# Kernel tuning notes

Hardware: AMD Instinct MI355X
Metric: run time of the kernel (lower is better)

The kernel has to match this reference:

```python
import jax, jax.numpy as jnp
import numpy as np

IN_DIM = 768
OUT_DIM = 128
N_NODES = 100000
N_EDGES = 1600000


def setup_inputs() -> dict:
    key = jax.random.key(0)
    ks = jax.random.split(key, 9)
    features = jax.random.normal(ks[0], (N_NODES, IN_DIM), dtype=jnp.float32)
    src = jax.random.randint(ks[1], (N_EDGES,), 0, N_NODES, dtype=jnp.int32)
    dst = jax.random.randint(ks[2], (N_EDGES,), 0, N_NODES, dtype=jnp.int32)
    s = 1.0 / np.sqrt(IN_DIM)
    Wd = jax.random.uniform(ks[3], (IN_DIM, OUT_DIM), jnp.float32, -s, s)
    bd = jax.random.uniform(ks[4], (OUT_DIM,), jnp.float32, -s, s)
    sg = 1.0 / np.sqrt(OUT_DIM)
    Wg = jax.random.uniform(ks[5], (OUT_DIM, OUT_DIM), jnp.float32, -sg, sg)
    bg = jnp.zeros((OUT_DIM,), jnp.float32)  # DGL GraphConv bias init: zeros
    Wu = jax.random.uniform(ks[6], (OUT_DIM, 768), jnp.float32, -sg, sg)
    bu = jax.random.uniform(ks[7], (768,), jnp.float32, -sg, sg)
    return {"features": features, "Wd": Wd, "bd": bd, "Wg": Wg, "bg": bg,
            "Wu": Wu, "bu": bu, "src": src, "dst": dst}


def reference(features, Wd, bd, Wg, bg, Wu, bu, src, dst):
    # down-projection: [N, in_dim] -> [N, out_dim]
    h = features @ Wd + bd

    # DGL GraphConv, norm='both': D_in^{-1/2} A D_out^{-1/2} (h W) + b
    ones = jnp.ones_like(src, dtype=h.dtype)
    out_deg = jax.ops.segment_sum(ones, src, num_segments=N_NODES)
    in_deg = jax.ops.segment_sum(ones, dst, num_segments=N_NODES)
    norm_src = jax.lax.rsqrt(jnp.maximum(out_deg, 1.0))  # clamp(min=1)
    norm_dst = jax.lax.rsqrt(jnp.maximum(in_deg, 1.0))

    # in_feats == out_feats -> aggregate first, then multiply by Wg
    h = h * norm_src[:, None]
    agg = jax.ops.segment_sum(h[src], dst, num_segments=N_NODES)  # [N, out_dim]
    agg = agg * norm_dst[:, None]
    g = agg @ Wg + bg

    # up-projection back to 768
    return g @ Wu + bu
```

## Files before the change

kernel.cpp:

```cpp
#include <hip/hip_runtime.h>
#include <cstdint>
#include <cstddef>

#define IN_DIM 768
#define OUT_DIM 128
#define N_NODES 100000
#define N_EDGES 1600000

typedef __bf16 bf16x8 __attribute__((ext_vector_type(8)));
typedef float f32x4 __attribute__((ext_vector_type(4)));

static __device__ __forceinline__ unsigned short f2bf(float f) {
  unsigned u = __builtin_bit_cast(unsigned, f);
  u += 0x7fffu + ((u >> 16) & 1u);
  return (unsigned short)(u >> 16);
}
static __device__ __forceinline__ float bflo(unsigned u) {
  return __builtin_bit_cast(float, u << 16);
}
static __device__ __forceinline__ float bfhi(unsigned u) {
  return __builtin_bit_cast(float, u & 0xffff0000u);
}


__global__ void deg_kernel(const int* __restrict__ src, const int* __restrict__ dst,
                           int* __restrict__ out_deg, int* __restrict__ in_deg) {
  int e = blockIdx.x * 256 + threadIdx.x;
  if (e < N_EDGES) {
    atomicAdd(&out_deg[src[e]], 1);
    atomicAdd(&in_deg[dst[e]], 1);
  }
}

__global__ void norm_kernel(const int* __restrict__ out_deg, float* __restrict__ norm_src) {
  int i = blockIdx.x * 256 + threadIdx.x;
  if (i < N_NODES) norm_src[i] = rsqrtf(fmaxf((float)out_deg[i], 1.0f));
}

__global__ __launch_bounds__(256) void scanA_kernel(const int* __restrict__ in_deg,
                                                    int* __restrict__ row_start,
                                                    int* __restrict__ blk_sums) {
  __shared__ int sm[256];
  const int tid = threadIdx.x;
  const int base = blockIdx.x * 1024;
  int idx = base + tid * 4;
  int v0 = (idx + 0 < N_NODES) ? in_deg[idx + 0] : 0;
  int v1 = (idx + 1 < N_NODES) ? in_deg[idx + 1] : 0;
  int v2 = (idx + 2 < N_NODES) ? in_deg[idx + 2] : 0;
  int v3 = (idx + 3 < N_NODES) ? in_deg[idx + 3] : 0;
  int t0 = v0, t1 = t0 + v1, t2 = t1 + v2, t3 = t2 + v3;
  sm[tid] = t3;
  __syncthreads();
  for (int off = 1; off < 256; off <<= 1) {
    int x = (tid >= off) ? sm[tid - off] : 0;
    __syncthreads();
    sm[tid] += x;
    __syncthreads();
  }
  int base_sum = tid ? sm[tid - 1] : 0;
  if (idx + 0 < N_NODES) row_start[idx + 0] = base_sum;
  if (idx + 1 < N_NODES) row_start[idx + 1] = base_sum + t0;
  if (idx + 2 < N_NODES) row_start[idx + 2] = base_sum + t1;
  if (idx + 3 < N_NODES) row_start[idx + 3] = base_sum + t2;
  if (tid == 255) blk_sums[blockIdx.x] = sm[255];
}

__global__ void scanB_kernel(const int* __restrict__ blk_sums, int* __restrict__ blk_off) {
  __shared__ int sm[128];
  const int tid = threadIdx.x;
  const int nblk = (N_NODES + 1023) / 1024;
  int v = (tid < nblk) ? blk_sums[tid] : 0;
  sm[tid] = v;
  __syncthreads();
  for (int off = 1; off < 128; off <<= 1) {
    int x = (tid >= off) ? sm[tid - off] : 0;
    __syncthreads();
    sm[tid] += x;
    __syncthreads();
  }
  blk_off[tid] = tid ? sm[tid - 1] : 0;
}

__global__ void scanC_kernel(int* __restrict__ row_start, const int* __restrict__ blk_off,
                             int* __restrict__ cursor) {
  int i = blockIdx.x * 256 + threadIdx.x;
  if (i < N_NODES) {
    int v = row_start[i] + blk_off[i >> 10];
    row_start[i] = v;
    cursor[i] = v;
  }
  if (i == 0) row_start[N_NODES] = N_EDGES;
}

__global__ void scatter_kernel(const int* __restrict__ src, const int* __restrict__ dst,
                               int* __restrict__ cursor, int* __restrict__ edge_src) {
  int e = blockIdx.x * 256 + threadIdx.x;
  if (e < N_EDGES) {
    int p = atomicAdd(&cursor[dst[e]], 1);
    edge_src[p] = src[e];
  }
}


__global__ void wdt_kernel(const float* __restrict__ Wd, unsigned short* __restrict__ WdT) {
  int n = blockIdx.x;
  int k = threadIdx.x;
  WdT[(size_t)n * IN_DIM + k] = f2bf(Wd[(size_t)k * OUT_DIM + n]);
}


__global__ __launch_bounds__(256) void gemm1_kernel(
    const float* __restrict__ feat, const unsigned short* __restrict__ WdT,
    const float* __restrict__ bd, const float* __restrict__ norm_src,
    unsigned short* __restrict__ hbf) {
  __shared__ unsigned short a_lds[64][72];
  __shared__ unsigned short b_lds[128][72];
  const int tid = threadIdx.x;
  const int wave = tid >> 6;
  const int lane = tid & 63;
  const int mrow = (wave >> 1) * 32;
  const int ncol = (wave & 1) * 64;
  const int block_m = blockIdx.x * 64;
  const int fm = lane & 15;
  const int fq = lane >> 4;

  f32x4 acc[2][4] = {};

  for (int k0 = 0; k0 < IN_DIM; k0 += 64) {
#pragma unroll
    for (int p = 0; p < 4; ++p) {
      int idx = tid + p * 256;
      int r = idx >> 4;
      int c4 = (idx & 15) * 4;
      int gr = block_m + r;
      float4 v;
      if (gr < N_NODES) v = *(const float4*)(feat + (size_t)gr * IN_DIM + k0 + c4);
      else v = make_float4(0.f, 0.f, 0.f, 0.f);
      ushort4 s;
      s.x = f2bf(v.x); s.y = f2bf(v.y); s.z = f2bf(v.z); s.w = f2bf(v.w);
      *(ushort4*)&a_lds[r][c4] = s;
    }
#pragma unroll
    for (int p = 0; p < 4; ++p) {
      int idx = tid + p * 256;
      int n = idx >> 3;
      int ch = (idx & 7) * 8;
      uint4 v = *(const uint4*)(WdT + (size_t)n * IN_DIM + k0 + ch);
      *(uint4*)&b_lds[n][ch] = v;
    }
    __syncthreads();
#pragma unroll
    for (int ks = 0; ks < 64; ks += 32) {
      int kc = ks + fq * 8;
      bf16x8 af[2], bfr[4];
      af[0] = *(const bf16x8*)&a_lds[mrow + fm][kc];
      af[1] = *(const bf16x8*)&a_lds[mrow + 16 + fm][kc];
#pragma unroll
      for (int i = 0; i < 4; ++i)
        bfr[i] = *(const bf16x8*)&b_lds[ncol + i * 16 + fm][kc];
#pragma unroll
      for (int mi = 0; mi < 2; ++mi)
#pragma unroll
        for (int ni = 0; ni < 4; ++ni)
          acc[mi][ni] = __builtin_amdgcn_mfma_f32_16x16x32_bf16(af[mi], bfr[ni], acc[mi][ni], 0, 0, 0);
    }
    __syncthreads();
  }
  const int fr = fq * 4;
#pragma unroll
  for (int mi = 0; mi < 2; ++mi) {
#pragma unroll
    for (int r = 0; r < 4; ++r) {
      int row = block_m + mrow + mi * 16 + fr + r;
      if (row < N_NODES) {
        float ns = norm_src[row];
#pragma unroll
        for (int ni = 0; ni < 4; ++ni) {
          int col = ncol + ni * 16 + fm;
          float val = (acc[mi][ni][r] + bd[col]) * ns;
          hbf[(size_t)row * OUT_DIM + col] = f2bf(val);
        }
      }
    }
  }
}


__global__ __launch_bounds__(256) void agg_kernel(
    const unsigned short* __restrict__ hbf, const int* __restrict__ row_start,
    const int* __restrict__ edge_src, unsigned short* __restrict__ aggb) {
  const int wave = threadIdx.x >> 6;
  const int lane = threadIdx.x & 63;
  const int v = blockIdx.x * 4 + wave;
  if (v >= N_NODES) return;
  const int beg = row_start[v];
  const int end = row_start[v + 1];
  const unsigned* hp = (const unsigned*)hbf;
  float a0 = 0.f, a1 = 0.f;
  for (int c = beg; c < end; c += 64) {
    int rem = end - c;
    int n = rem < 64 ? rem : 64;
    int sv = (c + lane < end) ? edge_src[c + lane] : 0;
    int j = 0;
    for (; j + 4 <= n; j += 4) {
      int s0 = __shfl(sv, j + 0);
      int s1 = __shfl(sv, j + 1);
      int s2 = __shfl(sv, j + 2);
      int s3 = __shfl(sv, j + 3);
      unsigned u0 = hp[(size_t)s0 * 64 + lane];
      unsigned u1 = hp[(size_t)s1 * 64 + lane];
      unsigned u2 = hp[(size_t)s2 * 64 + lane];
      unsigned u3 = hp[(size_t)s3 * 64 + lane];
      a0 += (bflo(u0) + bflo(u1)) + (bflo(u2) + bflo(u3));
      a1 += (bfhi(u0) + bfhi(u1)) + (bfhi(u2) + bfhi(u3));
    }
    for (; j < n; ++j) {
      int s = __shfl(sv, j);
      unsigned u = hp[(size_t)s * 64 + lane];
      a0 += bflo(u);
      a1 += bfhi(u);
    }
  }
  float nd = rsqrtf(fmaxf((float)(end - beg), 1.0f));
  a0 *= nd; a1 *= nd;
  unsigned o = (unsigned)f2bf(a0) | ((unsigned)f2bf(a1) << 16);
  ((unsigned*)aggb)[(size_t)v * 64 + lane] = o;
}


__global__ void wgu_kernel(const float* __restrict__ Wg, const float* __restrict__ Wu,
                           unsigned short* __restrict__ WguT) {
  int i = blockIdx.x * 256 + threadIdx.x;
  if (i >= 128 * 768) return;
  int r = i / 768, c = i % 768;
  float s = 0.f;
  for (int k = 0; k < 128; ++k) s += Wg[r * 128 + k] * Wu[(size_t)k * 768 + c];
  WguT[(size_t)c * 128 + r] = f2bf(s);
}

__global__ void bgu_kernel(const float* __restrict__ bg, const float* __restrict__ Wu,
                           const float* __restrict__ bu, float* __restrict__ bgu) {
  int c = blockIdx.x * 256 + threadIdx.x;
  if (c >= 768) return;
  float s = bu[c];
  for (int k = 0; k < 128; ++k) s += bg[k] * Wu[(size_t)k * 768 + c];
  bgu[c] = s;
}


__global__ __launch_bounds__(256) void gemm3_kernel(
    const unsigned short* __restrict__ aggb, const unsigned short* __restrict__ WguT,
    const float* __restrict__ bgu, float* __restrict__ out) {
  __shared__ unsigned short a_lds[128][72];
  __shared__ unsigned short b_lds[128][72];
  const int tid = threadIdx.x;
  const int wave = tid >> 6;
  const int lane = tid & 63;
  const int m_off = (wave >> 1) * 64;
  const int n_off = (wave & 1) * 64;
  const int block_m = blockIdx.x * 128;
  const int block_n = blockIdx.y * 128;
  const int fm = lane & 15;
  const int fq = lane >> 4;

  f32x4 acc[4][4] = {};

  for (int k0 = 0; k0 < 128; k0 += 64) {
#pragma unroll
    for (int p = 0; p < 4; ++p) {
      int idx = tid + p * 256;
      int r = idx >> 3, ch = idx & 7;
      int gr = block_m + r;
      uint4 v;
      if (gr < N_NODES) v = *(const uint4*)(aggb + (size_t)gr * 128 + k0 + ch * 8);
      else v = make_uint4(0u, 0u, 0u, 0u);
      *(uint4*)&a_lds[r][ch * 8] = v;
    }
#pragma unroll
    for (int p = 0; p < 4; ++p) {
      int idx = tid + p * 256;
      int n = idx >> 3, ch = idx & 7;
      uint4 v = *(const uint4*)(WguT + (size_t)(block_n + n) * 128 + k0 + ch * 8);
      *(uint4*)&b_lds[n][ch * 8] = v;
    }
    __syncthreads();
#pragma unroll
    for (int ks = 0; ks < 64; ks += 32) {
      bf16x8 af[4], bfr[4];
      int kc = ks + fq * 8;
#pragma unroll
      for (int i = 0; i < 4; ++i) af[i] = *(const bf16x8*)&a_lds[m_off + i * 16 + fm][kc];
#pragma unroll
      for (int i = 0; i < 4; ++i) bfr[i] = *(const bf16x8*)&b_lds[n_off + i * 16 + fm][kc];
#pragma unroll
      for (int mi = 0; mi < 4; ++mi)
#pragma unroll
        for (int ni = 0; ni < 4; ++ni)
          acc[mi][ni] = __builtin_amdgcn_mfma_f32_16x16x32_bf16(af[mi], bfr[ni], acc[mi][ni], 0, 0, 0);
    }
    __syncthreads();
  }
  const int fr = fq * 4;
#pragma unroll
  for (int mi = 0; mi < 4; ++mi) {
#pragma unroll
    for (int r = 0; r < 4; ++r) {
      int row = block_m + m_off + mi * 16 + fr + r;
      if (row < N_NODES) {
#pragma unroll
        for (int ni = 0; ni < 4; ++ni) {
          int col = block_n + n_off + ni * 16 + fm;
          out[(size_t)row * IN_DIM + col] = acc[mi][ni][r] + bgu[col];
        }
      }
    }
  }
}


extern "C" void kernel_launch(void* const* d_in, const int* in_sizes, int n_in,
                              void* d_out, int out_size, void* d_ws, size_t ws_size,
                              hipStream_t stream) {
  (void)in_sizes; (void)n_in; (void)out_size; (void)ws_size;
  const float* feat = (const float*)d_in[0];
  const float* Wd   = (const float*)d_in[1];
  const float* bd   = (const float*)d_in[2];
  const float* Wg   = (const float*)d_in[3];
  const float* bg   = (const float*)d_in[4];
  const float* Wu   = (const float*)d_in[5];
  const float* bu   = (const float*)d_in[6];
  const int*   src  = (const int*)d_in[7];
  const int*   dst  = (const int*)d_in[8];
  float* out = (float*)d_out;

  char* ws = (char*)d_ws;
  unsigned short* hbf       = (unsigned short*)(ws + 0);
  unsigned short* aggb      = (unsigned short*)(ws + 25600000);
  int*            edge_srcs = (int*)(ws + 51200000);
  int*            out_deg   = (int*)(ws + 57600000);
  int*            in_deg    = (int*)(ws + 58000000);
  int*            row_start = (int*)(ws + 58400000);
  int*            cursor    = (int*)(ws + 58800128);
  float*          norm_src  = (float*)(ws + 59200128);
  unsigned short* WguT      = (unsigned short*)(ws + 59600128);
  float*          bgu       = (float*)(ws + 59796736);
  unsigned short* WdT       = (unsigned short*)(ws + 59799808);
  int*            blk_sums  = (int*)(ws + 59996416);
  int*            blk_off   = (int*)(ws + 59996928);

  hipMemsetAsync(out_deg, 0, 800000, stream);
  deg_kernel<<<(N_EDGES + 255) / 256, 256, 0, stream>>>(src, dst, out_deg, in_deg);
  norm_kernel<<<(N_NODES + 255) / 256, 256, 0, stream>>>(out_deg, norm_src);
  scanA_kernel<<<(N_NODES + 1023) / 1024, 256, 0, stream>>>(in_deg, row_start, blk_sums);
  scanB_kernel<<<1, 128, 0, stream>>>(blk_sums, blk_off);
  scanC_kernel<<<(N_NODES + 255) / 256, 256, 0, stream>>>(row_start, blk_off, cursor);
  scatter_kernel<<<(N_EDGES + 255) / 256, 256, 0, stream>>>(src, dst, cursor, edge_srcs);
  wdt_kernel<<<128, 768, 0, stream>>>(Wd, WdT);
  gemm1_kernel<<<(N_NODES + 63) / 64, 256, 0, stream>>>(feat, WdT, bd, norm_src, hbf);
  agg_kernel<<<(N_NODES + 3) / 4, 256, 0, stream>>>(hbf, row_start, edge_srcs, aggb);
  wgu_kernel<<<(128 * 768 + 255) / 256, 256, 0, stream>>>(Wg, Wu, WguT);
  bgu_kernel<<<3, 256, 0, stream>>>(bg, Wu, bu, bgu);
  gemm3_kernel<<<dim3((N_NODES + 127) / 128, 6), 256, 0, stream>>>(aggb, WguT, bgu, out);
}
```

Before: 926.5 us.

## Prefetch global tiles into registers in GEMMs, widen gather unroll, remap gemm3 across XCDs

gemm1 and gemm3 now load the next K tile from global memory into registers while the current tile is used from LDS, which hides load latency. The agg kernel gathers 8 neighbour rows per step with predicated weights, replacing the 4-way loop plus scalar tail. gemm3 moves to a 1D grid whose block IDs are remapped so that consecutive tiles land on the same XCD, improving L2 locality. norm_kernel is dropped and the source norm is computed inline from out_deg in gemm1's epilogue. The price is more register pressure and some redundant loads on short tail chunks in agg.

```diff
diff --git a/kernel.cpp b/kernel.cpp
--- a/kernel.cpp
+++ b/kernel.cpp
@@ -30,11 +30,6 @@
     atomicAdd(&out_deg[src[e]], 1);
     atomicAdd(&in_deg[dst[e]], 1);
   }
-}
-
-__global__ void norm_kernel(const int* __restrict__ out_deg, float* __restrict__ norm_src) {
-  int i = blockIdx.x * 256 + threadIdx.x;
-  if (i < N_NODES) norm_src[i] = rsqrtf(fmaxf((float)out_deg[i], 1.0f));
 }
 
 __global__ __launch_bounds__(256) void scanA_kernel(const int* __restrict__ in_deg,
@@ -111,7 +106,7 @@
 
 __global__ __launch_bounds__(256) void gemm1_kernel(
     const float* __restrict__ feat, const unsigned short* __restrict__ WdT,
-    const float* __restrict__ bd, const float* __restrict__ norm_src,
+    const float* __restrict__ bd, const int* __restrict__ out_deg,
     unsigned short* __restrict__ hbf) {
   __shared__ unsigned short a_lds[64][72];
   __shared__ unsigned short b_lds[128][72];
@@ -124,31 +119,48 @@
   const int fm = lane & 15;
   const int fq = lane >> 4;
 
+  const int ar = tid >> 4;
+  const int ac4 = (tid & 15) * 4;
+  const int bn = tid >> 3;
+  const int bch = (tid & 7) * 8;
+
   f32x4 acc[2][4] = {};
+  float4 av[4];
+  uint4 bv[4];
+
+#pragma unroll
+  for (int p = 0; p < 4; ++p) {
+    int gr = block_m + ar + p * 16;
+    av[p] = (gr < N_NODES) ? *(const float4*)(feat + (size_t)gr * IN_DIM + ac4)
+                           : make_float4(0.f, 0.f, 0.f, 0.f);
+  }
+#pragma unroll
+  for (int p = 0; p < 4; ++p)
+    bv[p] = *(const uint4*)(WdT + (size_t)(bn + p * 32) * IN_DIM + bch);
 
   for (int k0 = 0; k0 < IN_DIM; k0 += 64) {
 #pragma unroll
     for (int p = 0; p < 4; ++p) {
-      int idx = tid + p * 256;
-      int r = idx >> 4;
-      int c4 = (idx & 15) * 4;
-      int gr = block_m + r;
-      float4 v;
-      if (gr < N_NODES) v = *(const float4*)(feat + (size_t)gr * IN_DIM + k0 + c4);
-      else v = make_float4(0.f, 0.f, 0.f, 0.f);
       ushort4 s;
-      s.x = f2bf(v.x); s.y = f2bf(v.y); s.z = f2bf(v.z); s.w = f2bf(v.w);
-      *(ushort4*)&a_lds[r][c4] = s;
-    }
-#pragma unroll
-    for (int p = 0; p < 4; ++p) {
-      int idx = tid + p * 256;
-      int n = idx >> 3;
-      int ch = (idx & 7) * 8;
-      uint4 v = *(const uint4*)(WdT + (size_t)n * IN_DIM + k0 + ch);
-      *(uint4*)&b_lds[n][ch] = v;
-    }
-    __syncthreads();
+      s.x = f2bf(av[p].x); s.y = f2bf(av[p].y); s.z = f2bf(av[p].z); s.w = f2bf(av[p].w);
+      *(ushort4*)&a_lds[ar + p * 16][ac4] = s;
+    }
+#pragma unroll
+    for (int p = 0; p < 4; ++p)
+      *(uint4*)&b_lds[bn + p * 32][bch] = bv[p];
+    __syncthreads();
+    int kn = k0 + 64;
+    if (kn < IN_DIM) {
+#pragma unroll
+      for (int p = 0; p < 4; ++p) {
+        int gr = block_m + ar + p * 16;
+        av[p] = (gr < N_NODES) ? *(const float4*)(feat + (size_t)gr * IN_DIM + kn + ac4)
+                               : make_float4(0.f, 0.f, 0.f, 0.f);
+      }
+#pragma unroll
+      for (int p = 0; p < 4; ++p)
+        bv[p] = *(const uint4*)(WdT + (size_t)(bn + p * 32) * IN_DIM + kn + bch);
+    }
 #pragma unroll
     for (int ks = 0; ks < 64; ks += 32) {
       int kc = ks + fq * 8;
@@ -173,7 +185,7 @@
     for (int r = 0; r < 4; ++r) {
       int row = block_m + mrow + mi * 16 + fr + r;
       if (row < N_NODES) {
-        float ns = norm_src[row];
+        float ns = rsqrtf(fmaxf((float)out_deg[row], 1.0f));
 #pragma unroll
         for (int ni = 0; ni < 4; ++ni) {
           int col = ncol + ni * 16 + fm;
@@ -201,24 +213,40 @@
     int rem = end - c;
     int n = rem < 64 ? rem : 64;
     int sv = (c + lane < end) ? edge_src[c + lane] : 0;
-    int j = 0;
-    for (; j + 4 <= n; j += 4) {
-      int s0 = __shfl(sv, j + 0);
-      int s1 = __shfl(sv, j + 1);
-      int s2 = __shfl(sv, j + 2);
-      int s3 = __shfl(sv, j + 3);
+    int l = n - 1;
+    for (int j = 0; j < n; j += 8) {
+      int j1 = j + 1, j2 = j + 2, j3 = j + 3, j4 = j + 4, j5 = j + 5, j6 = j + 6, j7 = j + 7;
+      int s0 = __shfl(sv, j);
+      int s1 = __shfl(sv, j1 < n ? j1 : l);
+      int s2 = __shfl(sv, j2 < n ? j2 : l);
+      int s3 = __shfl(sv, j3 < n ? j3 : l);
+      int s4 = __shfl(sv, j4 < n ? j4 : l);
+      int s5 = __shfl(sv, j5 < n ? j5 : l);
+      int s6 = __shfl(sv, j6 < n ? j6 : l);
+      int s7 = __shfl(sv, j7 < n ? j7 : l);
       unsigned u0 = hp[(size_t)s0 * 64 + lane];
       unsigned u1 = hp[(size_t)s1 * 64 + lane];
       unsigned u2 = hp[(size_t)s2 * 64 + lane];
       unsigned u3 = hp[(size_t)s3 * 64 + lane];
-      a0 += (bflo(u0) + bflo(u1)) + (bflo(u2) + bflo(u3));
-      a1 += (bfhi(u0) + bfhi(u1)) + (bfhi(u2) + bfhi(u3));
-    }
-    for (; j < n; ++j) {
-      int s = __shfl(sv, j);
-      unsigned u = hp[(size_t)s * 64 + lane];
-      a0 += bflo(u);
-      a1 += bfhi(u);
+      unsigned u4 = hp[(size_t)s4 * 64 + lane];
+      unsigned u5 = hp[(size_t)s5 * 64 + lane];
+      unsigned u6 = hp[(size_t)s6 * 64 + lane];
+      unsigned u7 = hp[(size_t)s7 * 64 + lane];
+      float w1 = j1 < n ? 1.f : 0.f;
+      float w2 = j2 < n ? 1.f : 0.f;
+      float w3 = j3 < n ? 1.f : 0.f;
+      float w4 = j4 < n ? 1.f : 0.f;
+      float w5 = j5 < n ? 1.f : 0.f;
+      float w6 = j6 < n ? 1.f : 0.f;
+      float w7 = j7 < n ? 1.f : 0.f;
+      a0 += bflo(u0);            a1 += bfhi(u0);
+      a0 = fmaf(w1, bflo(u1), a0); a1 = fmaf(w1, bfhi(u1), a1);
+      a0 = fmaf(w2, bflo(u2), a0); a1 = fmaf(w2, bfhi(u2), a1);
+      a0 = fmaf(w3, bflo(u3), a0); a1 = fmaf(w3, bfhi(u3), a1);
+      a0 = fmaf(w4, bflo(u4), a0); a1 = fmaf(w4, bfhi(u4), a1);
+      a0 = fmaf(w5, bflo(u5), a0); a1 = fmaf(w5, bfhi(u5), a1);
+      a0 = fmaf(w6, bflo(u6), a0); a1 = fmaf(w6, bfhi(u6), a1);
+      a0 = fmaf(w7, bflo(u7), a0); a1 = fmaf(w7, bfhi(u7), a1);
     }
   }
   float nd = rsqrtf(fmaxf((float)(end - beg), 1.0f));
@@ -258,32 +286,49 @@
   const int lane = tid & 63;
   const int m_off = (wave >> 1) * 64;
   const int n_off = (wave & 1) * 64;
-  const int block_m = blockIdx.x * 128;
-  const int block_n = blockIdx.y * 128;
+  const int nwg = ((N_NODES + 127) / 128) * 6;
+  int orig = blockIdx.x;
+  int q = nwg >> 3, r8 = nwg & 7;
+  int xcd = orig & 7, off = orig >> 3;
+  int wgid = (xcd < r8 ? xcd * (q + 1) : r8 * (q + 1) + (xcd - r8) * q) + off;
+  const int block_m = (wgid / 6) * 128;
+  const int block_n = (wgid % 6) * 128;
   const int fm = lane & 15;
   const int fq = lane >> 4;
 
+  const int sr = tid >> 3;
+  const int sch = (tid & 7) * 8;
+
   f32x4 acc[4][4] = {};
+  uint4 avv[4], bvv[4];
+
+#pragma unroll
+  for (int p = 0; p < 4; ++p) {
+    int rr = sr + p * 32;
+    int gr = block_m + rr;
+    avv[p] = (gr < N_NODES) ? *(const uint4*)(aggb + (size_t)gr * 128 + sch)
+                            : make_uint4(0u, 0u, 0u, 0u);
+    bvv[p] = *(const uint4*)(WguT + (size_t)(block_n + rr) * 128 + sch);
+  }
 
   for (int k0 = 0; k0 < 128; k0 += 64) {
 #pragma unroll
     for (int p = 0; p < 4; ++p) {
-      int idx = tid + p * 256;
-      int r = idx >> 3, ch = idx & 7;
-      int gr = block_m + r;
-      uint4 v;
-      if (gr < N_NODES) v = *(const uint4*)(aggb + (size_t)gr * 128 + k0 + ch * 8);
-      else v = make_uint4(0u, 0u, 0u, 0u);
-      *(uint4*)&a_lds[r][ch * 8] = v;
-    }
-#pragma unroll
-    for (int p = 0; p < 4; ++p) {
-      int idx = tid + p * 256;
-      int n = idx >> 3, ch = idx & 7;
-      uint4 v = *(const uint4*)(WguT + (size_t)(block_n + n) * 128 + k0 + ch * 8);
-      *(uint4*)&b_lds[n][ch * 8] = v;
-    }
-    __syncthreads();
+      int rr = sr + p * 32;
+      *(uint4*)&a_lds[rr][sch] = avv[p];
+      *(uint4*)&b_lds[rr][sch] = bvv[p];
+    }
+    __syncthreads();
+    if (k0 == 0) {
+#pragma unroll
+      for (int p = 0; p < 4; ++p) {
+        int rr = sr + p * 32;
+        int gr = block_m + rr;
+        avv[p] = (gr < N_NODES) ? *(const uint4*)(aggb + (size_t)gr * 128 + 64 + sch)
+                                : make_uint4(0u, 0u, 0u, 0u);
+        bvv[p] = *(const uint4*)(WguT + (size_t)(block_n + rr) * 128 + 64 + sch);
+      }
+    }
 #pragma unroll
     for (int ks = 0; ks < 64; ks += 32) {
       bf16x8 af[4], bfr[4];
@@ -341,7 +386,6 @@
   int*            in_deg    = (int*)(ws + 58000000);
   int*            row_start = (int*)(ws + 58400000);
   int*            cursor    = (int*)(ws + 58800128);
-  float*          norm_src  = (float*)(ws + 59200128);
   unsigned short* WguT      = (unsigned short*)(ws + 59600128);
   float*          bgu       = (float*)(ws + 59796736);
   unsigned short* WdT       = (unsigned short*)(ws + 59799808);
@@ -350,15 +394,14 @@
 
   hipMemsetAsync(out_deg, 0, 800000, stream);
   deg_kernel<<<(N_EDGES + 255) / 256, 256, 0, stream>>>(src, dst, out_deg, in_deg);
-  norm_kernel<<<(N_NODES + 255) / 256, 256, 0, stream>>>(out_deg, norm_src);
   scanA_kernel<<<(N_NODES + 1023) / 1024, 256, 0, stream>>>(in_deg, row_start, blk_sums);
   scanB_kernel<<<1, 128, 0, stream>>>(blk_sums, blk_off);
   scanC_kernel<<<(N_NODES + 255) / 256, 256, 0, stream>>>(row_start, blk_off, cursor);
   scatter_kernel<<<(N_EDGES + 255) / 256, 256, 0, stream>>>(src, dst, cursor, edge_srcs);
   wdt_kernel<<<128, 768, 0, stream>>>(Wd, WdT);
-  gemm1_kernel<<<(N_NODES + 63) / 64, 256, 0, stream>>>(feat, WdT, bd, norm_src, hbf);
+  gemm1_kernel<<<(N_NODES + 63) / 64, 256, 0, stream>>>(feat, WdT, bd, out_deg, hbf);
   agg_kernel<<<(N_NODES + 3) / 4, 256, 0, stream>>>(hbf, row_start, edge_srcs, aggb);
   wgu_kernel<<<(128 * 768 + 255) / 256, 256, 0, stream>>>(Wg, Wu, WguT);
   bgu_kernel<<<3, 256, 0, stream>>>(bg, Wu, bu, bgu);
-  gemm3_kernel<<<dim3((N_NODES + 127) / 128, 6), 256, 0, stream>>>(aggb, WguT, bgu, out);
-}
+  gemm3_kernel<<<((N_NODES + 127) / 128) * 6, 256, 0, stream>>>(aggb, WguT, bgu, out);
+}
```

New measurement: 997.1 us. 1.08x slower.
